# Kernel optimization log

Measured on AMD Instinct MI355X. Metric: run time of the kernel, lower is better.

The kernel has to match this reference:

```python
import jax, jax.numpy as jnp
import numpy as np

B, L, D, H, NL = 4, 2048, 512, 8, 2
HD = D // H  # 64
EPS = 1e-5


def _rotate_half(t):
    a, b = jnp.split(t, 2, axis=-1)
    return jnp.concatenate([-b, a], axis=-1)


def _ln(x, w, b):
    mu = jnp.mean(x, axis=-1, keepdims=True)
    var = jnp.mean((x - mu) ** 2, axis=-1, keepdims=True)
    return (x - mu) * jax.lax.rsqrt(var + EPS) * w + b


def setup_inputs() -> dict:
    key = jax.random.key(0)
    ks = jax.random.split(key, 8)
    x = jax.random.normal(ks[0], (B, L, D), dtype=jnp.float32)
    # 1D RoPE built per head_dim, tiled across heads -> [B, L, D]
    pos = jnp.arange(L, dtype=jnp.float32)
    inv_freq = 10000.0 ** (-2.0 * jnp.arange(HD, dtype=jnp.float32) / HD)
    theta = pos[:, None] * inv_freq[None, :]  # [L, HD]
    pos_cos = jnp.broadcast_to(jnp.tile(jnp.cos(theta), (1, H))[None], (B, L, D)).astype(jnp.float32)
    pos_sin = jnp.broadcast_to(jnp.tile(jnp.sin(theta), (1, H))[None], (B, L, D)).astype(jnp.float32)
    attn_mask = jnp.zeros((B, L), dtype=jnp.float32)  # all tokens valid
    s = 0.02
    Wq = s * jax.random.normal(ks[1], (NL, D, D), dtype=jnp.float32)
    Wk = s * jax.random.normal(ks[2], (NL, D, D), dtype=jnp.float32)
    Wv = s * jax.random.normal(ks[3], (NL, D, D), dtype=jnp.float32)
    Wo = s * jax.random.normal(ks[4], (NL, D, D), dtype=jnp.float32)
    W1 = s * jax.random.normal(ks[5], (NL, D, 2 * D), dtype=jnp.float32)
    W2 = s * jax.random.normal(ks[6], (NL, D, D), dtype=jnp.float32)
    ln1_w = jnp.ones((NL, D), jnp.float32); ln1_b = jnp.zeros((NL, D), jnp.float32)
    ln2_w = jnp.ones((NL, D), jnp.float32); ln2_b = jnp.zeros((NL, D), jnp.float32)
    lnf_w = jnp.ones((D,), jnp.float32); lnf_b = jnp.zeros((D,), jnp.float32)
    return dict(x=x, pos_cos=pos_cos, pos_sin=pos_sin, attn_mask=attn_mask,
                Wq=Wq, Wk=Wk, Wv=Wv, Wo=Wo, W1=W1, W2=W2,
                ln1_w=ln1_w, ln1_b=ln1_b, ln2_w=ln2_w, ln2_b=ln2_b,
                lnf_w=lnf_w, lnf_b=lnf_b)


def reference(x, pos_cos, pos_sin, attn_mask, Wq, Wk, Wv, Wo, W1, W2,
              ln1_w, ln1_b, ln2_w, ln2_b, lnf_w, lnf_b):
    # [B, H, L, HD]
    cos = pos_cos.reshape(B, L, H, HD).transpose(0, 2, 1, 3)
    sin = pos_sin.reshape(B, L, H, HD).transpose(0, 2, 1, 3)
    mask = attn_mask[:, None, None, :]  # [B,1,1,L]
    scale = 1.0 / np.float32(np.sqrt(HD))
    for i in range(NL):
        xn = _ln(x, ln1_w[i], ln1_b[i])
        q = (xn @ Wq[i]).reshape(B, L, H, HD).transpose(0, 2, 1, 3)
        k = (xn @ Wk[i]).reshape(B, L, H, HD).transpose(0, 2, 1, 3)
        v = (xn @ Wv[i]).reshape(B, L, H, HD).transpose(0, 2, 1, 3)
        q = q * cos + _rotate_half(q) * sin
        k = k * cos + _rotate_half(k) * sin
        scores = jnp.einsum('bhqd,bhkd->bhqk', q, k) * scale + mask
        probs = jax.nn.softmax(scores, axis=-1)
        ctx = jnp.einsum('bhqk,bhkd->bhqd', probs, v)
        ctx = ctx.transpose(0, 2, 1, 3).reshape(B, L, D)
        x = x + ctx @ Wo[i]
        xn = _ln(x, ln2_w[i], ln2_b[i])
        h = xn @ W1[i]
        x1, x2 = jnp.split(h, 2, axis=-1)
        x = x + (jax.nn.silu(x1) * x2) @ W2[i]
    return _ln(x, lnf_w, lnf_b)
```

## Files before the change

### kernel.cpp

```cpp
#include <hip/hip_runtime.h>

#define BB 4
#define LL 2048
#define DD 512
#define HH 8
#define NLAYER 2

typedef __attribute__((ext_vector_type(8))) short short8;
typedef __attribute__((ext_vector_type(4))) float floatx4;
typedef __attribute__((ext_vector_type(16))) float floatx16;

union U4S8 { uint4 u4; short8 s8; unsigned int u[4]; };

__device__ __forceinline__ unsigned short f2bf(float f) {
  unsigned int u = __float_as_uint(f);
  u += 0x7fffu + ((u >> 16) & 1u);
  return (unsigned short)(u >> 16);
}
__device__ __forceinline__ float bf2f(unsigned short s) {
  return __uint_as_float(((unsigned int)s) << 16);
}
__device__ __forceinline__ unsigned int pack_bf16(float a0, float a1) {
  unsigned int u0 = __float_as_uint(a0) + 0x8000u;
  unsigned int u1 = __float_as_uint(a1) + 0x8000u;
  return __builtin_amdgcn_perm(u1, u0, 0x07060302u);
}
__device__ __forceinline__ unsigned int pack_bf16_trunc(float a0, float a1) {
  return __builtin_amdgcn_perm(__float_as_uint(a1), __float_as_uint(a0), 0x07060302u);
}
__device__ __forceinline__ float fast_exp2(float x) {
#if __has_builtin(__builtin_amdgcn_exp2f)
  return __builtin_amdgcn_exp2f(x);
#else
  return exp2f(x);
#endif
}
__device__ __forceinline__ float fast_exp(float x) {
  return fast_exp2(x * 1.442695040888963f);
}

struct TJob { const float* src; unsigned short* dst; int C; int il; };
struct TJobs { TJob j[12]; };

__global__ __launch_bounds__(256) void transpose_all_kernel(TJobs jobs) {
  TJob jb = jobs.j[blockIdx.z];
  int c0 = blockIdx.x * 32;
  if (c0 >= jb.C) return;
  const int R = 512;
  __shared__ float t[32][33];
  int r0 = blockIdx.y * 32;
#pragma unroll
  for (int i = 0; i < 4; i++) {
    int idx = threadIdx.x + i * 256;
    t[idx >> 5][idx & 31] = jb.src[(size_t)(r0 + (idx >> 5)) * jb.C + c0 + (idx & 31)];
  }
  __syncthreads();
#pragma unroll
  for (int i = 0; i < 4; i++) {
    int idx = threadIdx.x + i * 256;
    int cc = idx >> 5, rr = idx & 31;
    int c = c0 + cc;
    int orow = jb.il ? ((c < 512) ? 2 * c : 2 * (c - 512) + 1) : c;
    jb.dst[(size_t)orow * R + r0 + rr] = f2bf(t[rr][cc]);
  }
}

__global__ __launch_bounds__(256) void ln_kernel(
    const float* __restrict__ x, const float* __restrict__ w, const float* __restrict__ b,
    unsigned short* __restrict__ outB, float* __restrict__ outF) {
  int row = blockIdx.x;
  const float* xr = x + (size_t)row * DD;
  int tid = threadIdx.x;
  float2 v = *(const float2*)(xr + tid * 2);
  float s = v.x + v.y;
  float ss = v.x * v.x + v.y * v.y;
#pragma unroll
  for (int off = 1; off < 64; off <<= 1) {
    s += __shfl_xor(s, off);
    ss += __shfl_xor(ss, off);
  }
  __shared__ float red[2][4];
  int wave = tid >> 6, lane = tid & 63;
  if (lane == 0) { red[0][wave] = s; red[1][wave] = ss; }
  __syncthreads();
  s = red[0][0] + red[0][1] + red[0][2] + red[0][3];
  ss = red[1][0] + red[1][1] + red[1][2] + red[1][3];
  float mu = s * (1.0f / DD);
  float var = ss * (1.0f / DD) - mu * mu;
  float inv = rsqrtf(var + 1e-5f);
#pragma unroll
  for (int j = 0; j < 2; j++) {
    int c = tid * 2 + j;
    float val = (((j == 0) ? v.x : v.y) - mu) * inv * w[c] + b[c];
    if (outB) outB[(size_t)row * DD + c] = f2bf(val);
    if (outF) outF[(size_t)row * DD + c] = val;
  }
}

__global__ __launch_bounds__(256) void gemm128_kernel(
    const unsigned short* __restrict__ A, const unsigned short* __restrict__ Bt,
    float* __restrict__ outF, unsigned short* __restrict__ outB,
    const float* __restrict__ res, int M, int N, int K) {
  __shared__ alignas(16) unsigned short As[128 * 32];
  __shared__ alignas(16) unsigned short Bs[128 * 32];
  const int tid = threadIdx.x;
  const int wave = tid >> 6, lane = tid & 63;
  const int l16 = lane & 15, quad = lane >> 4;
  const int wm = wave & 1, wn = wave >> 1;
  const int m0 = blockIdx.y * 128, n0 = blockIdx.x * 128;

  floatx4 acc[4][4];
#pragma unroll
  for (int i = 0; i < 4; i++)
#pragma unroll
    for (int j = 0; j < 4; j++)
#pragma unroll
      for (int r = 0; r < 4; r++) acc[i][j][r] = 0.f;

  const int grow = lane >> 2;
  const int gg = lane & 3;

  for (int kt = 0; kt < K; kt += 32) {
#pragma unroll
    for (int i = 0; i < 2; i++) {
      int rb = (wave * 2 + i) * 16;
      int row = rb + grow;
      int gsw = gg ^ (row & 3);
      const unsigned short* srcA = A + (size_t)(m0 + row) * K + kt + gsw * 8;
      const unsigned short* srcB = Bt + (size_t)(n0 + row) * K + kt + gsw * 8;
      __builtin_amdgcn_global_load_lds(
          (const __attribute__((address_space(1))) unsigned int*)srcA,
          (__attribute__((address_space(3))) unsigned int*)(As + rb * 32), 16, 0, 0);
      __builtin_amdgcn_global_load_lds(
          (const __attribute__((address_space(1))) unsigned int*)srcB,
          (__attribute__((address_space(3))) unsigned int*)(Bs + rb * 32), 16, 0, 0);
    }
    __syncthreads();
    short8 af[4], bf[4];
#pragma unroll
    for (int i = 0; i < 4; i++) {
      int rowa = wm * 64 + i * 16 + l16;
      af[i] = *(const short8*)&As[rowa * 32 + (quad ^ (rowa & 3)) * 8];
      int rowb = wn * 64 + i * 16 + l16;
      bf[i] = *(const short8*)&Bs[rowb * 32 + (quad ^ (rowb & 3)) * 8];
    }
#pragma unroll
    for (int i = 0; i < 4; i++)
#pragma unroll
      for (int j = 0; j < 4; j++)
        acc[i][j] = __builtin_amdgcn_mfma_f32_16x16x32_bf16(af[i], bf[j], acc[i][j], 0, 0, 0);
    __syncthreads();
  }
#pragma unroll
  for (int i = 0; i < 4; i++)
#pragma unroll
    for (int j = 0; j < 4; j++)
#pragma unroll
      for (int r = 0; r < 4; r++) {
        int row = m0 + wm * 64 + i * 16 + quad * 4 + r;
        int col = n0 + wn * 64 + j * 16 + l16;
        size_t idx = (size_t)row * N + col;
        float val = acc[i][j][r];
        if (res) val += res[idx];
        if (outF) outF[idx] = val;
        if (outB) outB[idx] = f2bf(val);
      }
}

__global__ __launch_bounds__(256) void gemm64n_kernel(
    const unsigned short* __restrict__ A, const unsigned short* __restrict__ Bt,
    float* __restrict__ outF, const float* __restrict__ res, int M, int N, int K) {
  __shared__ alignas(16) unsigned short As[128 * 32];
  __shared__ alignas(16) unsigned short Bs[64 * 32];
  const int tid = threadIdx.x;
  const int wave = tid >> 6, lane = tid & 63;
  const int l16 = lane & 15, quad = lane >> 4;
  const int m0 = blockIdx.y * 128, n0 = blockIdx.x * 64;

  floatx4 acc[2][4];
#pragma unroll
  for (int i = 0; i < 2; i++)
#pragma unroll
    for (int j = 0; j < 4; j++)
#pragma unroll
      for (int r = 0; r < 4; r++) acc[i][j][r] = 0.f;

  const int grow = lane >> 2;
  const int gg = lane & 3;

  for (int kt = 0; kt < K; kt += 32) {
#pragma unroll
    for (int i = 0; i < 3; i++) {
      int id = wave * 3 + i;
      if (id < 8) {
        int rb = id * 16;
        int row = rb + grow;
        int gsw = gg ^ (row & 3);
        const unsigned short* srcA = A + (size_t)(m0 + row) * K + kt + gsw * 8;
        __builtin_amdgcn_global_load_lds(
            (const __attribute__((address_space(1))) unsigned int*)srcA,
            (__attribute__((address_space(3))) unsigned int*)(As + rb * 32), 16, 0, 0);
      } else {
        int rb = (id - 8) * 16;
        int row = rb + grow;
        int gsw = gg ^ (row & 3);
        const unsigned short* srcB = Bt + (size_t)(n0 + row) * K + kt + gsw * 8;
        __builtin_amdgcn_global_load_lds(
            (const __attribute__((address_space(1))) unsigned int*)srcB,
            (__attribute__((address_space(3))) unsigned int*)(Bs + rb * 32), 16, 0, 0);
      }
    }
    __syncthreads();
    short8 af[2], bfr[4];
#pragma unroll
    for (int i = 0; i < 2; i++) {
      int rowa = wave * 32 + i * 16 + l16;
      af[i] = *(const short8*)&As[rowa * 32 + (quad ^ (rowa & 3)) * 8];
    }
#pragma unroll
    for (int j = 0; j < 4; j++) {
      int rowb = j * 16 + l16;
      bfr[j] = *(const short8*)&Bs[rowb * 32 + (quad ^ (rowb & 3)) * 8];
    }
#pragma unroll
    for (int i = 0; i < 2; i++)
#pragma unroll
      for (int j = 0; j < 4; j++)
        acc[i][j] = __builtin_amdgcn_mfma_f32_16x16x32_bf16(af[i], bfr[j], acc[i][j], 0, 0, 0);
    __syncthreads();
  }
#pragma unroll
  for (int i = 0; i < 2; i++)
#pragma unroll
    for (int j = 0; j < 4; j++)
#pragma unroll
      for (int r = 0; r < 4; r++) {
        int row = m0 + wave * 32 + i * 16 + quad * 4 + r;
        int col = n0 + j * 16 + l16;
        size_t idx = (size_t)row * N + col;
        float val = acc[i][j][r];
        if (res) val += res[idx];
        outF[idx] = val;
      }
}

__global__ __launch_bounds__(256) void gemm_swiglu_kernel(
    const unsigned short* __restrict__ A, const unsigned short* __restrict__ Bt,
    unsigned short* __restrict__ gout, int M, int N, int K) {
  __shared__ alignas(16) unsigned short As[128 * 32];
  __shared__ alignas(16) unsigned short Bs[128 * 32];
  const int tid = threadIdx.x;
  const int wave = tid >> 6, lane = tid & 63;
  const int l16 = lane & 15, quad = lane >> 4;
  const int wm = wave & 1, wn = wave >> 1;
  const int m0 = blockIdx.y * 128, n0 = blockIdx.x * 128;
  floatx4 acc[4][4];
#pragma unroll
  for (int i = 0; i < 4; i++)
#pragma unroll
    for (int j = 0; j < 4; j++)
#pragma unroll
      for (int r = 0; r < 4; r++) acc[i][j][r] = 0.f;
  const int grow = lane >> 2;
  const int gg = lane & 3;
  for (int kt = 0; kt < K; kt += 32) {
#pragma unroll
    for (int i = 0; i < 2; i++) {
      int rb = (wave * 2 + i) * 16;
      int row = rb + grow;
      int gsw = gg ^ (row & 3);
      const unsigned short* srcA = A + (size_t)(m0 + row) * K + kt + gsw * 8;
      const unsigned short* srcB = Bt + (size_t)(n0 + row) * K + kt + gsw * 8;
      __builtin_amdgcn_global_load_lds(
          (const __attribute__((address_space(1))) unsigned int*)srcA,
          (__attribute__((address_space(3))) unsigned int*)(As + rb * 32), 16, 0, 0);
      __builtin_amdgcn_global_load_lds(
          (const __attribute__((address_space(1))) unsigned int*)srcB,
          (__attribute__((address_space(3))) unsigned int*)(Bs + rb * 32), 16, 0, 0);
    }
    __syncthreads();
    short8 af[4], bf[4];
#pragma unroll
    for (int i = 0; i < 4; i++) {
      int rowa = wm * 64 + i * 16 + l16;
      af[i] = *(const short8*)&As[rowa * 32 + (quad ^ (rowa & 3)) * 8];
      int rowb = wn * 64 + i * 16 + l16;
      bf[i] = *(const short8*)&Bs[rowb * 32 + (quad ^ (rowb & 3)) * 8];
    }
#pragma unroll
    for (int i = 0; i < 4; i++)
#pragma unroll
      for (int j = 0; j < 4; j++)
        acc[i][j] = __builtin_amdgcn_mfma_f32_16x16x32_bf16(af[i], bf[j], acc[i][j], 0, 0, 0);
    __syncthreads();
  }
  const int Nh = N >> 1;
#pragma unroll
  for (int i = 0; i < 4; i++)
#pragma unroll
    for (int j = 0; j < 4; j++)
#pragma unroll
      for (int r = 0; r < 4; r++) {
        float val = acc[i][j][r];
        float part = __shfl_xor(val, 1);
        float x1 = (l16 & 1) ? part : val;
        float x2 = (l16 & 1) ? val : part;
        float g = x1 / (1.f + fast_exp(-x1)) * x2;
        if (!(l16 & 1)) {
          int row = m0 + wm * 64 + i * 16 + quad * 4 + r;
          int gcol = (n0 + wn * 64 + j * 16 + l16) >> 1;
          gout[(size_t)row * Nh + gcol] = f2bf(g);
        }
      }
}

__global__ __launch_bounds__(256) void ropevt_kernel(
    unsigned short* __restrict__ qkv, const float* __restrict__ cosb,
    const float* __restrict__ sinb, unsigned short* __restrict__ vtp) {
  __shared__ unsigned short tt[64][72];
  int lt = blockIdx.x, bh = blockIdx.y;
  int b = bh >> 3, h = bh & 7;
  int tid = threadIdx.x;
  {
    int r = tid >> 2, d0 = (tid & 3) * 8;
    size_t trow = (size_t)(b * LL + lt * 64 + r);
    const float* cp = cosb + (size_t)(lt * 64 + r) * DD + d0;
    const float* sp = sinb + (size_t)(lt * 64 + r) * DD + d0;
    unsigned short* qp = qkv + trow * 1536 + h * 64 + d0;
    unsigned short* kp = qp + 512;
    float4 c1a = *(const float4*)cp, c1b = *(const float4*)(cp + 4);
    float4 c2a = *(const float4*)(cp + 32), c2b = *(const float4*)(cp + 36);
    float4 s1a = *(const float4*)sp, s1b = *(const float4*)(sp + 4);
    float4 s2a = *(const float4*)(sp + 32), s2b = *(const float4*)(sp + 36);
    float c1[8] = {c1a.x, c1a.y, c1a.z, c1a.w, c1b.x, c1b.y, c1b.z, c1b.w};
    float c2[8] = {c2a.x, c2a.y, c2a.z, c2a.w, c2b.x, c2b.y, c2b.z, c2b.w};
    float s1[8] = {s1a.x, s1a.y, s1a.z, s1a.w, s1b.x, s1b.y, s1b.z, s1b.w};
    float s2[8] = {s2a.x, s2a.y, s2a.z, s2a.w, s2b.x, s2b.y, s2b.z, s2b.w};
    U4S8 qlo, qhi, klo, khi;
    qlo.u4 = *(const uint4*)qp; qhi.u4 = *(const uint4*)(qp + 32);
    klo.u4 = *(const uint4*)kp; khi.u4 = *(const uint4*)(kp + 32);
    U4S8 qlo2, qhi2, klo2, khi2;
#pragma unroll
    for (int e = 0; e < 4; e++) {
      float q1a = bf2f((unsigned short)qlo.s8[2 * e]), q1b = bf2f((unsigned short)qlo.s8[2 * e + 1]);
      float q2a = bf2f((unsigned short)qhi.s8[2 * e]), q2b = bf2f((unsigned short)qhi.s8[2 * e + 1]);
      qlo2.u[e] = pack_bf16(q1a * c1[2 * e] - q2a * s1[2 * e], q1b * c1[2 * e + 1] - q2b * s1[2 * e + 1]);
      qhi2.u[e] = pack_bf16(q2a * c2[2 * e] + q1a * s2[2 * e], q2b * c2[2 * e + 1] + q1b * s2[2 * e + 1]);
      float k1a = bf2f((unsigned short)klo.s8[2 * e]), k1b = bf2f((unsigned short)klo.s8[2 * e + 1]);
      float k2a = bf2f((unsigned short)khi.s8[2 * e]), k2b = bf2f((unsigned short)khi.s8[2 * e + 1]);
      klo2.u[e] = pack_bf16(k1a * c1[2 * e] - k2a * s1[2 * e], k1b * c1[2 * e + 1] - k2b * s1[2 * e + 1]);
      khi2.u[e] = pack_bf16(k2a * c2[2 * e] + k1a * s2[2 * e], k2b * c2[2 * e + 1] + k1b * s2[2 * e + 1]);
    }
    *(uint4*)qp = qlo2.u4; *(uint4*)(qp + 32) = qhi2.u4;
    *(uint4*)kp = klo2.u4; *(uint4*)(kp + 32) = khi2.u4;
  }
  {
    int row = tid >> 2, c = (tid & 3) * 16;
    const unsigned short* src = qkv + (size_t)(b * LL + lt * 64 + row) * 1536 + 1024 + h * 64 + c;
    *(uint4*)&tt[row][c] = *(const uint4*)src;
    *(uint4*)&tt[row][c + 8] = *(const uint4*)(src + 8);
    __syncthreads();
    int d = tid >> 2, lg = tid & 3;
    unsigned short arr[16];
#pragma unroll
    for (int i = 0; i < 16; i++) {
      int j = (i + d) & 15;
      arr[j] = tt[lg * 16 + j][d];
    }
    unsigned int w[8];
#pragma unroll
    for (int g = 0; g < 8; g++)
      w[g] = (unsigned int)arr[2 * g] | ((unsigned int)arr[2 * g + 1] << 16);
    unsigned short* dst = vtp + (size_t)(bh * 64 + d) * 2048 + lt * 64 + lg * 16;
    *(uint4*)dst = make_uint4(w[0], w[1], w[2], w[3]);
    *(uint4*)(dst + 8) = make_uint4(w[4], w[5], w[6], w[7]);
  }
}

__global__ __launch_bounds__(256, 2) void attn_kernel(
    const unsigned short* __restrict__ qkv, const unsigned short* __restrict__ vtp,
    const float* __restrict__ mask, unsigned short* __restrict__ ctx) {
  __shared__ alignas(16) unsigned short Ks[2][64][72];
  __shared__ alignas(16) unsigned short Vs[2][64][72];
  const int tid = threadIdx.x;
  const int wave = tid >> 6, lane = tid & 63;
  const int l5 = lane & 31, b5 = lane >> 5;
  const int b = blockIdx.z, h = blockIdx.y;
  const int q0 = blockIdx.x * 128 + wave * 32;
  const int bh = b * 8 + h;
  const float QSCALE = 0.125f * 1.442695040888963f;

  short8 qf[4];
  {
    const unsigned short* qp = qkv + (size_t)(b * LL + q0 + l5) * 1536 + h * 64 + b5 * 8;
#pragma unroll
    for (int t = 0; t < 4; t++) {
      U4S8 u;
      u.u4 = *(const uint4*)(qp + t * 16);
      short8 qs;
#pragma unroll
      for (int e = 0; e < 8; e++)
        qs[e] = (short)f2bf(bf2f((unsigned short)u.s8[e]) * QSCALE);
      qf[t] = qs;
    }
  }
  short8 bones = {0, 0, 0, 0, 0, 0, 0, 0};
  if (b5 == 0) bones[0] = (short)0x3F80;
  short8 onesA;
#pragma unroll
  for (int e = 0; e < 8; e++) onesA[e] = (short)0x3F80;

  floatx16 O[2], Lacc;
#pragma unroll
  for (int a = 0; a < 2; a++)
#pragma unroll
    for (int r = 0; r < 16; r++) O[a][r] = 0.f;
#pragma unroll
  for (int r = 0; r < 16; r++) Lacc[r] = 0.f;

  const int srow = tid >> 2, sc = (tid & 3) * 16;
  const unsigned short* kbase = qkv + (size_t)(b * LL + srow) * 1536 + 512 + h * 64 + sc;
  const unsigned short* vbase = vtp + (size_t)(bh * 64 + srow) * 2048 + sc;

  uint4 kr0 = *(const uint4*)kbase;
  uint4 kr1 = *(const uint4*)(kbase + 8);
  uint4 vr0 = *(const uint4*)vbase;
  uint4 vr1 = *(const uint4*)(vbase + 8);

  for (int t0 = 0, it = 0; t0 < LL; t0 += 64, it++) {
    const int buf = it & 1;
    *(uint4*)&Ks[buf][srow][sc] = kr0;
    *(uint4*)&Ks[buf][srow][sc + 8] = kr1;
    *(uint4*)&Vs[buf][srow][sc] = vr0;
    *(uint4*)&Vs[buf][srow][sc + 8] = vr1;
    __syncthreads();
    if (t0 + 64 < LL) {
      const unsigned short* kn = kbase + (size_t)(t0 + 64) * 1536;
      const unsigned short* vn = vbase + t0 + 64;
      kr0 = *(const uint4*)kn;
      kr1 = *(const uint4*)(kn + 8);
      vr0 = *(const uint4*)vn;
      vr1 = *(const uint4*)(vn + 8);
    }
    float mk0 = mask[b * LL + t0 + l5];
    float mk1 = mask[b * LL + t0 + 32 + l5];
    short8 am0 = {0, 0, 0, 0, 0, 0, 0, 0}, am1 = {0, 0, 0, 0, 0, 0, 0, 0};
    if (b5 == 0) {
      am0[0] = (short)f2bf(1.442695040888963f * mk0);
      am1[0] = (short)f2bf(1.442695040888963f * mk1);
    }
    short8 kf[2][4];
#pragma unroll
    for (int ms = 0; ms < 2; ms++)
#pragma unroll
      for (int t = 0; t < 4; t++)
        kf[ms][t] = *(const short8*)&Ks[buf][ms * 32 + l5][t * 16 + b5 * 8];

    floatx16 s0, s1;
#pragma unroll
    for (int r = 0; r < 16; r++) { s0[r] = 0.f; s1[r] = 0.f; }
#pragma unroll
    for (int t = 0; t < 4; t++) {
      s0 = __builtin_amdgcn_mfma_f32_32x32x16_bf16(kf[0][t], qf[t], s0, 0, 0, 0);
      s1 = __builtin_amdgcn_mfma_f32_32x32x16_bf16(kf[1][t], qf[t], s1, 0, 0, 0);
    }
    s0 = __builtin_amdgcn_mfma_f32_32x32x16_bf16(am0, bones, s0, 0, 0, 0);
    s1 = __builtin_amdgcn_mfma_f32_32x32x16_bf16(am1, bones, s1, 0, 0, 0);

    unsigned int pk[2][8];
#pragma unroll
    for (int i = 0; i < 8; i++) {
      pk[0][i] = pack_bf16_trunc(fast_exp2(s0[2 * i]), fast_exp2(s0[2 * i + 1]));
      pk[1][i] = pack_bf16_trunc(fast_exp2(s1[2 * i]), fast_exp2(s1[2 * i + 1]));
    }
#pragma unroll
    for (int ms = 0; ms < 2; ms++) {
#pragma unroll
      for (int kp = 0; kp < 2; kp++) {
        unsigned int se0 = b5 ? pk[ms][4 * kp] : pk[ms][4 * kp + 2];
        unsigned int se1 = b5 ? pk[ms][4 * kp + 1] : pk[ms][4 * kp + 3];
        unsigned int w0 = (unsigned int)__shfl_xor((int)se0, 32);
        unsigned int w1 = (unsigned int)__shfl_xor((int)se1, 32);
        U4S8 u;
        u.u[0] = b5 ? w0 : pk[ms][4 * kp];
        u.u[1] = b5 ? w1 : pk[ms][4 * kp + 1];
        u.u[2] = b5 ? pk[ms][4 * kp + 2] : w0;
        u.u[3] = b5 ? pk[ms][4 * kp + 3] : w1;
        short8 pb = u.s8;
        const int kst = ms * 2 + kp;
        short8 v0 = *(const short8*)&Vs[buf][l5][kst * 16 + b5 * 8];
        short8 v1 = *(const short8*)&Vs[buf][32 + l5][kst * 16 + b5 * 8];
        O[0] = __builtin_amdgcn_mfma_f32_32x32x16_bf16(v0, pb, O[0], 0, 0, 0);
        O[1] = __builtin_amdgcn_mfma_f32_32x32x16_bf16(v1, pb, O[1], 0, 0, 0);
        Lacc = __builtin_amdgcn_mfma_f32_32x32x16_bf16(onesA, pb, Lacc, 0, 0, 0);
      }
    }
  }
  float inv = 1.0f / Lacc[0];
  int qrow = q0 + l5;
  unsigned short* op = ctx + (size_t)(b * LL + qrow) * 512 + h * 64;
#pragma unroll
  for (int ds = 0; ds < 2; ds++) {
#pragma unroll
    for (int g = 0; g < 4; g++) {
      uint2 w;
      w.x = pack_bf16(O[ds][4 * g] * inv, O[ds][4 * g + 1] * inv);
      w.y = pack_bf16(O[ds][4 * g + 2] * inv, O[ds][4 * g + 3] * inv);
      *(uint2*)(op + ds * 32 + 8 * g + 4 * b5) = w;
    }
  }
}

extern "C" void kernel_launch(void* const* d_in, const int* in_sizes, int n_in,
                              void* d_out, int out_size, void* d_ws, size_t ws_size,
                              hipStream_t stream) {
  const float* x_in = (const float*)d_in[0];
  const float* pcos = (const float*)d_in[1];
  const float* psin = (const float*)d_in[2];
  const float* amask = (const float*)d_in[3];
  const float* Wq = (const float*)d_in[4];
  const float* Wk = (const float*)d_in[5];
  const float* Wv = (const float*)d_in[6];
  const float* Wo = (const float*)d_in[7];
  const float* W1 = (const float*)d_in[8];
  const float* W2 = (const float*)d_in[9];
  const float* ln1w = (const float*)d_in[10];
  const float* ln1b = (const float*)d_in[11];
  const float* ln2w = (const float*)d_in[12];
  const float* ln2b = (const float*)d_in[13];
  const float* lnfw = (const float*)d_in[14];
  const float* lnfb = (const float*)d_in[15];

  const int M = BB * LL;
  char* p = (char*)d_ws;
  float* x_ws = (float*)p;                  p += (size_t)M * DD * 4;
  unsigned short* xn = (unsigned short*)p;  p += (size_t)M * DD * 2;
  unsigned short* qkv = (unsigned short*)p; p += (size_t)M * 1536 * 2;
  unsigned short* vtb = (unsigned short*)p; p += (size_t)M * DD * 2;
  unsigned short* cb = (unsigned short*)p;  p += (size_t)M * DD * 2;
  unsigned short* wts = (unsigned short*)p;
  unsigned short* gb = vtb;

  const size_t LW = 786432 + 262144 + 524288 + 262144;
  TJobs jobs;
  for (int i = 0; i < NLAYER; i++) {
    unsigned short* wl = wts + i * LW;
    jobs.j[i * 6 + 0] = {Wq + (size_t)i * 262144, wl + 0, 512, 0};
    jobs.j[i * 6 + 1] = {Wk + (size_t)i * 262144, wl + 262144, 512, 0};
    jobs.j[i * 6 + 2] = {Wv + (size_t)i * 262144, wl + 524288, 512, 0};
    jobs.j[i * 6 + 3] = {Wo + (size_t)i * 262144, wl + 786432, 512, 0};
    jobs.j[i * 6 + 4] = {W1 + (size_t)i * 524288, wl + 1048576, 1024, 1};
    jobs.j[i * 6 + 5] = {W2 + (size_t)i * 262144, wl + 1572864, 512, 0};
  }
  transpose_all_kernel<<<dim3(32, 16, 12), 256, 0, stream>>>(jobs);

  for (int i = 0; i < NLAYER; i++) {
    unsigned short* wl = wts + i * LW;
    const float* xin = (i == 0) ? x_in : x_ws;
    ln_kernel<<<M, 256, 0, stream>>>(xin, ln1w + i * DD, ln1b + i * DD, xn, nullptr);
    gemm128_kernel<<<dim3(12, 64), 256, 0, stream>>>(xn, wl + 0, nullptr, qkv, nullptr, M, 1536, 512);
    ropevt_kernel<<<dim3(32, 32), 256, 0, stream>>>(qkv, pcos, psin, vtb);
    attn_kernel<<<dim3(LL / 128, HH, BB), 256, 0, stream>>>(qkv, vtb, amask, cb);
    gemm64n_kernel<<<dim3(8, 64), 256, 0, stream>>>(cb, wl + 786432, x_ws, xin, M, 512, 512);
    ln_kernel<<<M, 256, 0, stream>>>(x_ws, ln2w + i * DD, ln2b + i * DD, xn, nullptr);
    gemm_swiglu_kernel<<<dim3(8, 64), 256, 0, stream>>>(xn, wl + 1048576, gb, M, 1024, 512);
    gemm64n_kernel<<<dim3(8, 64), 256, 0, stream>>>(gb, wl + 1572864, x_ws, x_ws, M, 512, 512);
  }
  ln_kernel<<<M, 256, 0, stream>>>(x_ws, lnfw, lnfb, nullptr, (float*)d_out);
}
```

Baseline: 493.6 us.

## Split attention KV range in two and combine partial outputs

Result: slower. 524.8 us (+6.3%).

```diff
diff --git a/kernel.cpp b/kernel.cpp
--- a/kernel.cpp
+++ b/kernel.cpp
@@ -19,6 +19,12 @@
 }
 __device__ __forceinline__ float bf2f(unsigned short s) {
   return __uint_as_float(((unsigned int)s) << 16);
+}
+__device__ __forceinline__ float bf2f_lo(unsigned int w) {
+  return __uint_as_float(w << 16);
+}
+__device__ __forceinline__ float bf2f_hi(unsigned int w) {
+  return __uint_as_float(w & 0xffff0000u);
 }
 __device__ __forceinline__ unsigned int pack_bf16(float a0, float a1) {
   unsigned int u0 = __float_as_uint(a0) + 0x8000u;
@@ -377,17 +383,20 @@
   }
 }
 
-__global__ __launch_bounds__(256, 2) void attn_kernel(
+__global__ __launch_bounds__(256, 4) void attn_kernel(
     const unsigned short* __restrict__ qkv, const unsigned short* __restrict__ vtp,
-    const float* __restrict__ mask, unsigned short* __restrict__ ctx) {
+    const float* __restrict__ mask, unsigned short* __restrict__ opart0,
+    unsigned short* __restrict__ opart1, float* __restrict__ lpart) {
   __shared__ alignas(16) unsigned short Ks[2][64][72];
   __shared__ alignas(16) unsigned short Vs[2][64][72];
   const int tid = threadIdx.x;
   const int wave = tid >> 6, lane = tid & 63;
   const int l5 = lane & 31, b5 = lane >> 5;
-  const int b = blockIdx.z, h = blockIdx.y;
+  const int b = blockIdx.z >> 1, kz = blockIdx.z & 1;
+  const int h = blockIdx.y;
   const int q0 = blockIdx.x * 128 + wave * 32;
   const int bh = b * 8 + h;
+  const int kstart = kz << 10;
   const float QSCALE = 0.125f * 1.442695040888963f;
 
   short8 qf[4];
@@ -419,36 +428,31 @@
   for (int r = 0; r < 16; r++) Lacc[r] = 0.f;
 
   const int srow = tid >> 2, sc = (tid & 3) * 16;
-  const unsigned short* kbase = qkv + (size_t)(b * LL + srow) * 1536 + 512 + h * 64 + sc;
-  const unsigned short* vbase = vtp + (size_t)(bh * 64 + srow) * 2048 + sc;
+  const unsigned short* kbase = qkv + (size_t)(b * LL + kstart + srow) * 1536 + 512 + h * 64 + sc;
+  const unsigned short* vbase = vtp + (size_t)(bh * 64 + srow) * 2048 + kstart + sc;
 
   uint4 kr0 = *(const uint4*)kbase;
   uint4 kr1 = *(const uint4*)(kbase + 8);
   uint4 vr0 = *(const uint4*)vbase;
   uint4 vr1 = *(const uint4*)(vbase + 8);
 
-  for (int t0 = 0, it = 0; t0 < LL; t0 += 64, it++) {
+  for (int tl = 0, it = 0; tl < 1024; tl += 64, it++) {
     const int buf = it & 1;
     *(uint4*)&Ks[buf][srow][sc] = kr0;
     *(uint4*)&Ks[buf][srow][sc + 8] = kr1;
     *(uint4*)&Vs[buf][srow][sc] = vr0;
     *(uint4*)&Vs[buf][srow][sc + 8] = vr1;
     __syncthreads();
-    if (t0 + 64 < LL) {
-      const unsigned short* kn = kbase + (size_t)(t0 + 64) * 1536;
-      const unsigned short* vn = vbase + t0 + 64;
+    if (tl + 64 < 1024) {
+      const unsigned short* kn = kbase + (size_t)(tl + 64) * 1536;
+      const unsigned short* vn = vbase + tl + 64;
       kr0 = *(const uint4*)kn;
       kr1 = *(const uint4*)(kn + 8);
       vr0 = *(const uint4*)vn;
       vr1 = *(const uint4*)(vn + 8);
     }
-    float mk0 = mask[b * LL + t0 + l5];
-    float mk1 = mask[b * LL + t0 + 32 + l5];
-    short8 am0 = {0, 0, 0, 0, 0, 0, 0, 0}, am1 = {0, 0, 0, 0, 0, 0, 0, 0};
-    if (b5 == 0) {
-      am0[0] = (short)f2bf(1.442695040888963f * mk0);
-      am1[0] = (short)f2bf(1.442695040888963f * mk1);
-    }
+    float mk0 = mask[b * LL + kstart + tl + l5];
+    float mk1 = mask[b * LL + kstart + tl + 32 + l5];
     short8 kf[2][4];
 #pragma unroll
     for (int ms = 0; ms < 2; ms++)
@@ -464,8 +468,15 @@
       s0 = __builtin_amdgcn_mfma_f32_32x32x16_bf16(kf[0][t], qf[t], s0, 0, 0, 0);
       s1 = __builtin_amdgcn_mfma_f32_32x32x16_bf16(kf[1][t], qf[t], s1, 0, 0, 0);
     }
-    s0 = __builtin_amdgcn_mfma_f32_32x32x16_bf16(am0, bones, s0, 0, 0, 0);
-    s1 = __builtin_amdgcn_mfma_f32_32x32x16_bf16(am1, bones, s1, 0, 0, 0);
+    if (__any(mk0 != 0.0f || mk1 != 0.0f)) {
+      short8 am0 = {0, 0, 0, 0, 0, 0, 0, 0}, am1 = {0, 0, 0, 0, 0, 0, 0, 0};
+      if (b5 == 0) {
+        am0[0] = (short)f2bf(1.442695040888963f * mk0);
+        am1[0] = (short)f2bf(1.442695040888963f * mk1);
+      }
+      s0 = __builtin_amdgcn_mfma_f32_32x32x16_bf16(am0, bones, s0, 0, 0, 0);
+      s1 = __builtin_amdgcn_mfma_f32_32x32x16_bf16(am1, bones, s1, 0, 0, 0);
+    }
 
     unsigned int pk[2][8];
 #pragma unroll
@@ -496,19 +507,41 @@
       }
     }
   }
-  float inv = 1.0f / Lacc[0];
   int qrow = q0 + l5;
-  unsigned short* op = ctx + (size_t)(b * LL + qrow) * 512 + h * 64;
+  unsigned short* op = (kz ? opart1 : opart0) + (size_t)(b * LL + qrow) * 512 + h * 64;
 #pragma unroll
   for (int ds = 0; ds < 2; ds++) {
 #pragma unroll
     for (int g = 0; g < 4; g++) {
       uint2 w;
-      w.x = pack_bf16(O[ds][4 * g] * inv, O[ds][4 * g + 1] * inv);
-      w.y = pack_bf16(O[ds][4 * g + 2] * inv, O[ds][4 * g + 3] * inv);
+      w.x = pack_bf16(O[ds][4 * g], O[ds][4 * g + 1]);
+      w.y = pack_bf16(O[ds][4 * g + 2], O[ds][4 * g + 3]);
       *(uint2*)(op + ds * 32 + 8 * g + 4 * b5) = w;
     }
   }
+  if (b5 == 0) lpart[(size_t)(kz * 32 + bh) * 2048 + qrow] = Lacc[0];
+}
+
+__global__ __launch_bounds__(256) void attn_combine_kernel(
+    const unsigned short* o0, const unsigned short* o1,
+    const float* __restrict__ lp, unsigned short* out) {
+  int gtid = blockIdx.x * 256 + threadIdx.x;
+  int row = gtid >> 7;
+  int c = (gtid & 127) * 4;
+  int b = row >> 11, q = row & 2047, h = c >> 6;
+  int bh = b * 8 + h;
+  float L = lp[(size_t)bh * 2048 + q] + lp[(size_t)(32 + bh) * 2048 + q];
+  float inv = 1.0f / L;
+  uint2 a = *(const uint2*)&o0[(size_t)row * 512 + c];
+  uint2 bb = *(const uint2*)&o1[(size_t)row * 512 + c];
+  float e0 = (bf2f_lo(a.x) + bf2f_lo(bb.x)) * inv;
+  float e1 = (bf2f_hi(a.x) + bf2f_hi(bb.x)) * inv;
+  float e2 = (bf2f_lo(a.y) + bf2f_lo(bb.y)) * inv;
+  float e3 = (bf2f_hi(a.y) + bf2f_hi(bb.y)) * inv;
+  uint2 w;
+  w.x = pack_bf16(e0, e1);
+  w.y = pack_bf16(e2, e3);
+  *(uint2*)&out[(size_t)row * 512 + c] = w;
 }
 
 extern "C" void kernel_launch(void* const* d_in, const int* in_sizes, int n_in,
@@ -538,8 +571,11 @@
   unsigned short* qkv = (unsigned short*)p; p += (size_t)M * 1536 * 2;
   unsigned short* vtb = (unsigned short*)p; p += (size_t)M * DD * 2;
   unsigned short* cb = (unsigned short*)p;  p += (size_t)M * DD * 2;
+  float* lpart = (float*)p;                 p += (size_t)64 * 2048 * 4;
   unsigned short* wts = (unsigned short*)p;
   unsigned short* gb = vtb;
+  unsigned short* op0 = xn;
+  unsigned short* op1 = cb;
 
   const size_t LW = 786432 + 262144 + 524288 + 262144;
   TJobs jobs;
@@ -560,7 +596,8 @@
     ln_kernel<<<M, 256, 0, stream>>>(xin, ln1w + i * DD, ln1b + i * DD, xn, nullptr);
     gemm128_kernel<<<dim3(12, 64), 256, 0, stream>>>(xn, wl + 0, nullptr, qkv, nullptr, M, 1536, 512);
     ropevt_kernel<<<dim3(32, 32), 256, 0, stream>>>(qkv, pcos, psin, vtb);
-    attn_kernel<<<dim3(LL / 128, HH, BB), 256, 0, stream>>>(qkv, vtb, amask, cb);
+    attn_kernel<<<dim3(LL / 128, HH, BB * 2), 256, 0, stream>>>(qkv, vtb, amask, op0, op1, lpart);
+    attn_combine_kernel<<<(M * DD / 4) / 256, 256, 0, stream>>>(op0, op1, lpart, cb);
     gemm64n_kernel<<<dim3(8, 64), 256, 0, stream>>>(cb, wl + 786432, x_ws, xin, M, 512, 512);
     ln_kernel<<<M, 256, 0, stream>>>(x_ws, ln2w + i * DD, ln2b + i * DD, xn, nullptr);
     gemm_swiglu_kernel<<<dim3(8, 64), 256, 0, stream>>>(xn, wl + 1048576, gb, M, 1024, 512);
```

## Write V transposed from QKV GEMM epilogue and software-pipeline attention PV stage

Applied to the files above, without the earlier changes.

After: 477.6 us. 3.3% less time.

```diff
diff --git a/kernel.cpp b/kernel.cpp
--- a/kernel.cpp
+++ b/kernel.cpp
@@ -100,7 +100,8 @@
 __global__ __launch_bounds__(256) void gemm128_kernel(
     const unsigned short* __restrict__ A, const unsigned short* __restrict__ Bt,
     float* __restrict__ outF, unsigned short* __restrict__ outB,
-    const float* __restrict__ res, int M, int N, int K) {
+    const float* __restrict__ res, int M, int N, int K,
+    unsigned short* __restrict__ vtp) {
   __shared__ alignas(16) unsigned short As[128 * 32];
   __shared__ alignas(16) unsigned short Bs[128 * 32];
   const int tid = threadIdx.x;
@@ -150,6 +151,23 @@
       for (int j = 0; j < 4; j++)
         acc[i][j] = __builtin_amdgcn_mfma_f32_16x16x32_bf16(af[i], bf[j], acc[i][j], 0, 0, 0);
     __syncthreads();
+  }
+  if (vtp && n0 >= 1024) {
+#pragma unroll
+    for (int i = 0; i < 4; i++)
+#pragma unroll
+      for (int j = 0; j < 4; j++) {
+        int cg = (n0 - 1024) + wn * 64 + j * 16 + l16;
+        int hh = cg >> 6, dd = cg & 63;
+        int seq0 = m0 + wm * 64 + i * 16 + quad * 4;
+        int bI = seq0 >> 11, ls = seq0 & 2047;
+        unsigned short* dst = vtp + ((size_t)(bI * 8 + hh) * 64 + dd) * 2048 + ls;
+        uint2 w;
+        w.x = pack_bf16(acc[i][j][0], acc[i][j][1]);
+        w.y = pack_bf16(acc[i][j][2], acc[i][j][3]);
+        *(uint2*)dst = w;
+      }
+    return;
   }
 #pragma unroll
   for (int i = 0; i < 4; i++)
@@ -314,74 +332,50 @@
       }
 }
 
-__global__ __launch_bounds__(256) void ropevt_kernel(
+__global__ __launch_bounds__(256) void rope_kernel(
     unsigned short* __restrict__ qkv, const float* __restrict__ cosb,
-    const float* __restrict__ sinb, unsigned short* __restrict__ vtp) {
-  __shared__ unsigned short tt[64][72];
+    const float* __restrict__ sinb) {
   int lt = blockIdx.x, bh = blockIdx.y;
   int b = bh >> 3, h = bh & 7;
   int tid = threadIdx.x;
-  {
-    int r = tid >> 2, d0 = (tid & 3) * 8;
-    size_t trow = (size_t)(b * LL + lt * 64 + r);
-    const float* cp = cosb + (size_t)(lt * 64 + r) * DD + d0;
-    const float* sp = sinb + (size_t)(lt * 64 + r) * DD + d0;
-    unsigned short* qp = qkv + trow * 1536 + h * 64 + d0;
-    unsigned short* kp = qp + 512;
-    float4 c1a = *(const float4*)cp, c1b = *(const float4*)(cp + 4);
-    float4 c2a = *(const float4*)(cp + 32), c2b = *(const float4*)(cp + 36);
-    float4 s1a = *(const float4*)sp, s1b = *(const float4*)(sp + 4);
-    float4 s2a = *(const float4*)(sp + 32), s2b = *(const float4*)(sp + 36);
-    float c1[8] = {c1a.x, c1a.y, c1a.z, c1a.w, c1b.x, c1b.y, c1b.z, c1b.w};
-    float c2[8] = {c2a.x, c2a.y, c2a.z, c2a.w, c2b.x, c2b.y, c2b.z, c2b.w};
-    float s1[8] = {s1a.x, s1a.y, s1a.z, s1a.w, s1b.x, s1b.y, s1b.z, s1b.w};
-    float s2[8] = {s2a.x, s2a.y, s2a.z, s2a.w, s2b.x, s2b.y, s2b.z, s2b.w};
-    U4S8 qlo, qhi, klo, khi;
-    qlo.u4 = *(const uint4*)qp; qhi.u4 = *(const uint4*)(qp + 32);
-    klo.u4 = *(const uint4*)kp; khi.u4 = *(const uint4*)(kp + 32);
-    U4S8 qlo2, qhi2, klo2, khi2;
-#pragma unroll
-    for (int e = 0; e < 4; e++) {
-      float q1a = bf2f((unsigned short)qlo.s8[2 * e]), q1b = bf2f((unsigned short)qlo.s8[2 * e + 1]);
-      float q2a = bf2f((unsigned short)qhi.s8[2 * e]), q2b = bf2f((unsigned short)qhi.s8[2 * e + 1]);
-      qlo2.u[e] = pack_bf16(q1a * c1[2 * e] - q2a * s1[2 * e], q1b * c1[2 * e + 1] - q2b * s1[2 * e + 1]);
-      qhi2.u[e] = pack_bf16(q2a * c2[2 * e] + q1a * s2[2 * e], q2b * c2[2 * e + 1] + q1b * s2[2 * e + 1]);
-      float k1a = bf2f((unsigned short)klo.s8[2 * e]), k1b = bf2f((unsigned short)klo.s8[2 * e + 1]);
-      float k2a = bf2f((unsigned short)khi.s8[2 * e]), k2b = bf2f((unsigned short)khi.s8[2 * e + 1]);
-      klo2.u[e] = pack_bf16(k1a * c1[2 * e] - k2a * s1[2 * e], k1b * c1[2 * e + 1] - k2b * s1[2 * e + 1]);
-      khi2.u[e] = pack_bf16(k2a * c2[2 * e] + k1a * s2[2 * e], k2b * c2[2 * e + 1] + k1b * s2[2 * e + 1]);
-    }
-    *(uint4*)qp = qlo2.u4; *(uint4*)(qp + 32) = qhi2.u4;
-    *(uint4*)kp = klo2.u4; *(uint4*)(kp + 32) = khi2.u4;
-  }
-  {
-    int row = tid >> 2, c = (tid & 3) * 16;
-    const unsigned short* src = qkv + (size_t)(b * LL + lt * 64 + row) * 1536 + 1024 + h * 64 + c;
-    *(uint4*)&tt[row][c] = *(const uint4*)src;
-    *(uint4*)&tt[row][c + 8] = *(const uint4*)(src + 8);
-    __syncthreads();
-    int d = tid >> 2, lg = tid & 3;
-    unsigned short arr[16];
-#pragma unroll
-    for (int i = 0; i < 16; i++) {
-      int j = (i + d) & 15;
-      arr[j] = tt[lg * 16 + j][d];
-    }
-    unsigned int w[8];
-#pragma unroll
-    for (int g = 0; g < 8; g++)
-      w[g] = (unsigned int)arr[2 * g] | ((unsigned int)arr[2 * g + 1] << 16);
-    unsigned short* dst = vtp + (size_t)(bh * 64 + d) * 2048 + lt * 64 + lg * 16;
-    *(uint4*)dst = make_uint4(w[0], w[1], w[2], w[3]);
-    *(uint4*)(dst + 8) = make_uint4(w[4], w[5], w[6], w[7]);
-  }
+  int r = tid >> 2, d0 = (tid & 3) * 8;
+  size_t trow = (size_t)(b * LL + lt * 64 + r);
+  const float* cp = cosb + (size_t)(lt * 64 + r) * DD + d0;
+  const float* sp = sinb + (size_t)(lt * 64 + r) * DD + d0;
+  unsigned short* qp = qkv + trow * 1536 + h * 64 + d0;
+  unsigned short* kp = qp + 512;
+  float4 c1a = *(const float4*)cp, c1b = *(const float4*)(cp + 4);
+  float4 c2a = *(const float4*)(cp + 32), c2b = *(const float4*)(cp + 36);
+  float4 s1a = *(const float4*)sp, s1b = *(const float4*)(sp + 4);
+  float4 s2a = *(const float4*)(sp + 32), s2b = *(const float4*)(sp + 36);
+  float c1[8] = {c1a.x, c1a.y, c1a.z, c1a.w, c1b.x, c1b.y, c1b.z, c1b.w};
+  float c2[8] = {c2a.x, c2a.y, c2a.z, c2a.w, c2b.x, c2b.y, c2b.z, c2b.w};
+  float s1[8] = {s1a.x, s1a.y, s1a.z, s1a.w, s1b.x, s1b.y, s1b.z, s1b.w};
+  float s2[8] = {s2a.x, s2a.y, s2a.z, s2a.w, s2b.x, s2b.y, s2b.z, s2b.w};
+  U4S8 qlo, qhi, klo, khi;
+  qlo.u4 = *(const uint4*)qp; qhi.u4 = *(const uint4*)(qp + 32);
+  klo.u4 = *(const uint4*)kp; khi.u4 = *(const uint4*)(kp + 32);
+  U4S8 qlo2, qhi2, klo2, khi2;
+#pragma unroll
+  for (int e = 0; e < 4; e++) {
+    float q1a = bf2f((unsigned short)qlo.s8[2 * e]), q1b = bf2f((unsigned short)qlo.s8[2 * e + 1]);
+    float q2a = bf2f((unsigned short)qhi.s8[2 * e]), q2b = bf2f((unsigned short)qhi.s8[2 * e + 1]);
+    qlo2.u[e] = pack_bf16(q1a * c1[2 * e] - q2a * s1[2 * e], q1b * c1[2 * e + 1] - q2b * s1[2 * e + 1]);
+    qhi2.u[e] = pack_bf16(q2a * c2[2 * e] + q1a * s2[2 * e], q2b * c2[2 * e + 1] + q1b * s2[2 * e + 1]);
+    float k1a = bf2f((unsigned short)klo.s8[2 * e]), k1b = bf2f((unsigned short)klo.s8[2 * e + 1]);
+    float k2a = bf2f((unsigned short)khi.s8[2 * e]), k2b = bf2f((unsigned short)khi.s8[2 * e + 1]);
+    klo2.u[e] = pack_bf16(k1a * c1[2 * e] - k2a * s1[2 * e], k1b * c1[2 * e + 1] - k2b * s1[2 * e + 1]);
+    khi2.u[e] = pack_bf16(k2a * c2[2 * e] + k1a * s2[2 * e], k2b * c2[2 * e + 1] + k1b * s2[2 * e + 1]);
+  }
+  *(uint4*)qp = qlo2.u4; *(uint4*)(qp + 32) = qhi2.u4;
+  *(uint4*)kp = klo2.u4; *(uint4*)(kp + 32) = khi2.u4;
 }
 
 __global__ __launch_bounds__(256, 2) void attn_kernel(
     const unsigned short* __restrict__ qkv, const unsigned short* __restrict__ vtp,
     const float* __restrict__ mask, unsigned short* __restrict__ ctx) {
-  __shared__ alignas(16) unsigned short Ks[2][64][72];
-  __shared__ alignas(16) unsigned short Vs[2][64][72];
+  __shared__ alignas(16) unsigned short Ks[3][64][72];
+  __shared__ alignas(16) unsigned short Vs[3][64][72];
   const int tid = threadIdx.x;
   const int wave = tid >> 6, lane = tid & 63;
   const int l5 = lane & 31, b5 = lane >> 5;
@@ -427,51 +421,12 @@
   uint4 vr0 = *(const uint4*)vbase;
   uint4 vr1 = *(const uint4*)(vbase + 8);
 
-  for (int t0 = 0, it = 0; t0 < LL; t0 += 64, it++) {
-    const int buf = it & 1;
-    *(uint4*)&Ks[buf][srow][sc] = kr0;
-    *(uint4*)&Ks[buf][srow][sc + 8] = kr1;
-    *(uint4*)&Vs[buf][srow][sc] = vr0;
-    *(uint4*)&Vs[buf][srow][sc + 8] = vr1;
-    __syncthreads();
-    if (t0 + 64 < LL) {
-      const unsigned short* kn = kbase + (size_t)(t0 + 64) * 1536;
-      const unsigned short* vn = vbase + t0 + 64;
-      kr0 = *(const uint4*)kn;
-      kr1 = *(const uint4*)(kn + 8);
-      vr0 = *(const uint4*)vn;
-      vr1 = *(const uint4*)(vn + 8);
-    }
-    float mk0 = mask[b * LL + t0 + l5];
-    float mk1 = mask[b * LL + t0 + 32 + l5];
-    short8 am0 = {0, 0, 0, 0, 0, 0, 0, 0}, am1 = {0, 0, 0, 0, 0, 0, 0, 0};
-    if (b5 == 0) {
-      am0[0] = (short)f2bf(1.442695040888963f * mk0);
-      am1[0] = (short)f2bf(1.442695040888963f * mk1);
-    }
-    short8 kf[2][4];
-#pragma unroll
-    for (int ms = 0; ms < 2; ms++)
-#pragma unroll
-      for (int t = 0; t < 4; t++)
-        kf[ms][t] = *(const short8*)&Ks[buf][ms * 32 + l5][t * 16 + b5 * 8];
-
-    floatx16 s0, s1;
-#pragma unroll
-    for (int r = 0; r < 16; r++) { s0[r] = 0.f; s1[r] = 0.f; }
-#pragma unroll
-    for (int t = 0; t < 4; t++) {
-      s0 = __builtin_amdgcn_mfma_f32_32x32x16_bf16(kf[0][t], qf[t], s0, 0, 0, 0);
-      s1 = __builtin_amdgcn_mfma_f32_32x32x16_bf16(kf[1][t], qf[t], s1, 0, 0, 0);
-    }
-    s0 = __builtin_amdgcn_mfma_f32_32x32x16_bf16(am0, bones, s0, 0, 0, 0);
-    s1 = __builtin_amdgcn_mfma_f32_32x32x16_bf16(am1, bones, s1, 0, 0, 0);
-
+  auto do_pv = [&](const floatx16& a0, const floatx16& a1, int vb) {
     unsigned int pk[2][8];
 #pragma unroll
     for (int i = 0; i < 8; i++) {
-      pk[0][i] = pack_bf16_trunc(fast_exp2(s0[2 * i]), fast_exp2(s0[2 * i + 1]));
-      pk[1][i] = pack_bf16_trunc(fast_exp2(s1[2 * i]), fast_exp2(s1[2 * i + 1]));
+      pk[0][i] = pack_bf16_trunc(fast_exp2(a0[2 * i]), fast_exp2(a0[2 * i + 1]));
+      pk[1][i] = pack_bf16_trunc(fast_exp2(a1[2 * i]), fast_exp2(a1[2 * i + 1]));
     }
 #pragma unroll
     for (int ms = 0; ms < 2; ms++) {
@@ -488,14 +443,64 @@
         u.u[3] = b5 ? pk[ms][4 * kp + 3] : w1;
         short8 pb = u.s8;
         const int kst = ms * 2 + kp;
-        short8 v0 = *(const short8*)&Vs[buf][l5][kst * 16 + b5 * 8];
-        short8 v1 = *(const short8*)&Vs[buf][32 + l5][kst * 16 + b5 * 8];
+        short8 v0 = *(const short8*)&Vs[vb][l5][kst * 16 + b5 * 8];
+        short8 v1 = *(const short8*)&Vs[vb][32 + l5][kst * 16 + b5 * 8];
         O[0] = __builtin_amdgcn_mfma_f32_32x32x16_bf16(v0, pb, O[0], 0, 0, 0);
         O[1] = __builtin_amdgcn_mfma_f32_32x32x16_bf16(v1, pb, O[1], 0, 0, 0);
         Lacc = __builtin_amdgcn_mfma_f32_32x32x16_bf16(onesA, pb, Lacc, 0, 0, 0);
       }
     }
-  }
+  };
+
+  floatx16 sp0, sp1;
+  int buf = 0, pbuf = 0;
+  for (int it = 0; it < 32; it++) {
+    *(uint4*)&Ks[buf][srow][sc] = kr0;
+    *(uint4*)&Ks[buf][srow][sc + 8] = kr1;
+    *(uint4*)&Vs[buf][srow][sc] = vr0;
+    *(uint4*)&Vs[buf][srow][sc + 8] = vr1;
+    __syncthreads();
+    if (it < 31) {
+      const unsigned short* kn = kbase + (size_t)((it + 1) * 64) * 1536;
+      const unsigned short* vn = vbase + (it + 1) * 64;
+      kr0 = *(const uint4*)kn;
+      kr1 = *(const uint4*)(kn + 8);
+      vr0 = *(const uint4*)vn;
+      vr1 = *(const uint4*)(vn + 8);
+    }
+    int t0 = it * 64;
+    float mk0 = mask[b * LL + t0 + l5];
+    float mk1 = mask[b * LL + t0 + 32 + l5];
+    short8 kf[2][4];
+#pragma unroll
+    for (int ms = 0; ms < 2; ms++)
+#pragma unroll
+      for (int t = 0; t < 4; t++)
+        kf[ms][t] = *(const short8*)&Ks[buf][ms * 32 + l5][t * 16 + b5 * 8];
+
+    floatx16 s0, s1;
+#pragma unroll
+    for (int r = 0; r < 16; r++) { s0[r] = 0.f; s1[r] = 0.f; }
+#pragma unroll
+    for (int t = 0; t < 4; t++) {
+      s0 = __builtin_amdgcn_mfma_f32_32x32x16_bf16(kf[0][t], qf[t], s0, 0, 0, 0);
+      s1 = __builtin_amdgcn_mfma_f32_32x32x16_bf16(kf[1][t], qf[t], s1, 0, 0, 0);
+    }
+    if (__any(mk0 != 0.0f || mk1 != 0.0f)) {
+      short8 am0 = {0, 0, 0, 0, 0, 0, 0, 0}, am1 = {0, 0, 0, 0, 0, 0, 0, 0};
+      if (b5 == 0) {
+        am0[0] = (short)f2bf(1.442695040888963f * mk0);
+        am1[0] = (short)f2bf(1.442695040888963f * mk1);
+      }
+      s0 = __builtin_amdgcn_mfma_f32_32x32x16_bf16(am0, bones, s0, 0, 0, 0);
+      s1 = __builtin_amdgcn_mfma_f32_32x32x16_bf16(am1, bones, s1, 0, 0, 0);
+    }
+    if (it > 0) do_pv(sp0, sp1, pbuf);
+    sp0 = s0; sp1 = s1; pbuf = buf;
+    buf = (buf == 2) ? 0 : buf + 1;
+  }
+  do_pv(sp0, sp1, pbuf);
+
   float inv = 1.0f / Lacc[0];
   int qrow = q0 + l5;
   unsigned short* op = ctx + (size_t)(b * LL + qrow) * 512 + h * 64;
@@ -558,8 +563,8 @@
     unsigned short* wl = wts + i * LW;
     const float* xin = (i == 0) ? x_in : x_ws;
     ln_kernel<<<M, 256, 0, stream>>>(xin, ln1w + i * DD, ln1b + i * DD, xn, nullptr);
-    gemm128_kernel<<<dim3(12, 64), 256, 0, stream>>>(xn, wl + 0, nullptr, qkv, nullptr, M, 1536, 512);
-    ropevt_kernel<<<dim3(32, 32), 256, 0, stream>>>(qkv, pcos, psin, vtb);
+    gemm128_kernel<<<dim3(12, 64), 256, 0, stream>>>(xn, wl + 0, nullptr, qkv, nullptr, M, 1536, 512, vtb);
+    rope_kernel<<<dim3(32, 32), 256, 0, stream>>>(qkv, pcos, psin);
     attn_kernel<<<dim3(LL / 128, HH, BB), 256, 0, stream>>>(qkv, vtb, amask, cb);
     gemm64n_kernel<<<dim3(8, 64), 256, 0, stream>>>(cb, wl + 786432, x_ws, xin, M, 512, 512);
     ln_kernel<<<M, 256, 0, stream>>>(x_ws, ln2w + i * DD, ln2b + i * DD, xn, nullptr);
```
